# Performance work log

Measured on AMD Instinct MI355X. Metric: run time of the kernel, lower is better.

Reference implementation:

```python
import jax, jax.numpy as jnp
import numpy as np

EMBED = 1024
HEADS = 16
DK = EMBED // HEADS


def setup_inputs() -> dict:
    key = jax.random.key(0)
    ks = jax.random.split(key, 6)
    B, S = 2, 2048
    scale = 1.0 / np.sqrt(EMBED)
    x = jax.random.normal(ks[0], (B, S, EMBED), dtype=jnp.float32)
    Wq = jax.random.normal(ks[1], (EMBED, EMBED), dtype=jnp.float32) * scale
    Wk = jax.random.normal(ks[2], (EMBED, EMBED), dtype=jnp.float32) * scale
    Wv = jax.random.normal(ks[3], (EMBED, EMBED), dtype=jnp.float32) * scale
    Wo = jax.random.normal(ks[4], (EMBED, EMBED), dtype=jnp.float32) * scale
    qw = jnp.zeros((HEADS, 1), dtype=jnp.float32)  # quantum_weight, init quantum_scale=0
    return {"x": x, "Wq": Wq, "Wk": Wk, "Wv": Wv, "Wo": Wo, "qw": qw}


def reference(x, Wq, Wk, Wv, Wo, qw):
    B, S, E = x.shape
    # nn.Linear with no bias: y = x @ W.T; split heads -> [B,H,S,Dk]
    def proj(W):
        return (x @ W.T).reshape(B, S, HEADS, DK).transpose(0, 2, 1, 3)
    q, k, v = proj(Wq), proj(Wk), proj(Wv)
    scores = jnp.einsum('bhsd,bhtd->bhst', q, k) / np.sqrt(DK)
    attn = jax.nn.softmax(scores, axis=-1)  # dropout in eval mode: identity
    classical = jnp.einsum('bhst,bhtd->bhsd', attn, v)
    w = jax.nn.sigmoid(qw)[:, :, None]  # [H,1,1] per-head mixing weight
    out = w * jnp.sin(classical) + (1.0 - w) * classical
    out = out.transpose(0, 2, 1, 3).reshape(B, S, E)
    return out @ Wo.T
```

## Files before the change

### kernel.cpp

```cpp
#include <hip/hip_runtime.h>
#include <math.h>

constexpr int Ec  = 1024;
constexpr int Hc  = 16;
constexpr int DKc = 64;
constexpr int Bc  = 2;
constexpr int Sc  = 2048;
constexpr int Mc  = Bc * Sc;

typedef _Float16 half8 __attribute__((ext_vector_type(8)));
typedef _Float16 half4 __attribute__((ext_vector_type(4)));
typedef float    floatx4  __attribute__((ext_vector_type(4)));
typedef float    floatx16 __attribute__((ext_vector_type(16)));
typedef unsigned int uint2v __attribute__((ext_vector_type(2)));
typedef unsigned int uint4v __attribute__((ext_vector_type(4)));

#define MFMA16(a, b, c) __builtin_amdgcn_mfma_f32_16x16x32_f16(a, b, c, 0, 0, 0)
#define MFMA32(a, b, c) __builtin_amdgcn_mfma_f32_32x32x16_f16(a, b, c, 0, 0, 0)

__device__ __forceinline__ void async_lds16(const _Float16* g, _Float16* l)
{
    __builtin_amdgcn_global_load_lds(
        (const __attribute__((address_space(1))) unsigned int*)g,
        (__attribute__((address_space(3))) unsigned int*)l, 16, 0, 0);
}

__device__ __forceinline__ unsigned pkh2(float a, float b)
{
    return __builtin_bit_cast(unsigned, __builtin_amdgcn_cvt_pkrtz(a, b));
}

__global__ __launch_bounds__(256)
void convert_to_h(const float4* __restrict__ x,
                  const float4* __restrict__ wq,
                  const float4* __restrict__ wk,
                  const float4* __restrict__ wv,
                  const float4* __restrict__ wo,
                  half4* __restrict__ dst)
{
    const int i = blockIdx.x * 256 + threadIdx.x;
    const float4* src; int off;
    if      (i < 1048576) { src = x;  off = i; }
    else if (i < 1310720) { src = wq; off = i - 1048576; }
    else if (i < 1572864) { src = wk; off = i - 1310720; }
    else if (i < 1835008) { src = wv; off = i - 1572864; }
    else                  { src = wo; off = i - 1835008; }
    const float4 v = src[off];
    half4 o;
    o.x = (_Float16)v.x; o.y = (_Float16)v.y;
    o.z = (_Float16)v.z; o.w = (_Float16)v.w;
    dst[i] = o;
}

__device__ __forceinline__ void mfma_gemm_core64(const _Float16* __restrict__ A,
                                                 const _Float16* __restrict__ Bw,
                                                 int m0, int n0,
                                                 _Float16* As, _Float16* Bs,
                                                 floatx4 acc[4][4])
{
    const int tid  = threadIdx.x;
    const int wave = tid >> 6, lane = tid & 63;
    const int l16  = lane & 15, quad = lane >> 4;
    const int wrow = (wave >> 1) * 64, wcol = (wave & 1) * 64;

    const int srow8  = lane >> 3;
    const int schunk = (lane & 7) ^ (srow8 & 7);
    const _Float16* ga = A  + (size_t)(m0 + wave * 32 + srow8) * Ec + schunk * 8;
    const _Float16* gb = Bw + (size_t)(n0 + wave * 32 + srow8) * Ec + schunk * 8;
    _Float16* lA = As + (size_t)(wave * 32) * 64;
    _Float16* lB = Bs + (size_t)(wave * 32) * 64;

    for (int kt = 0; kt < Ec; kt += 64) {
#pragma unroll
        for (int c = 0; c < 4; ++c) {
            async_lds16(ga + (size_t)(c * 8) * Ec + kt, lA + c * 512);
            async_lds16(gb + (size_t)(c * 8) * Ec + kt, lB + c * 512);
        }
        __syncthreads();

        half8 af[4][2], bf[4][2];
#pragma unroll
        for (int i = 0; i < 4; ++i) {
            const int ra = wrow + i * 16 + l16;
            const int rb = wcol + i * 16 + l16;
#pragma unroll
            for (int kc = 0; kc < 2; ++kc) {
                af[i][kc] = *(const half8*)&As[ra * 64 + (((quad + kc * 4) ^ (ra & 7)) * 8)];
                bf[i][kc] = *(const half8*)&Bs[rb * 64 + (((quad + kc * 4) ^ (rb & 7)) * 8)];
            }
        }
#pragma unroll
        for (int i = 0; i < 4; ++i)
#pragma unroll
            for (int j = 0; j < 4; ++j) {
                acc[i][j] = MFMA16(af[i][0], bf[j][0], acc[i][j]);
                acc[i][j] = MFMA16(af[i][1], bf[j][1], acc[i][j]);
            }
        __syncthreads();
    }
}

__global__ __launch_bounds__(256)
void gemm_qkv_fused(const _Float16* __restrict__ xh,
                    const _Float16* __restrict__ wall,
                    _Float16* __restrict__ Qh,
                    _Float16* __restrict__ Kh,
                    _Float16* __restrict__ VTh)
{
    __shared__ __align__(16) _Float16 As[128 * 64];
    __shared__ __align__(16) _Float16 Bs[128 * 64];
    const int lin = blockIdx.x;
    const int swz = (lin & 7) * 96 + (lin >> 3);
    const int m0  = (swz / 24) * 128;
    const int n0f = (swz % 24) * 128;

    floatx4 acc[4][4] = {};
    mfma_gemm_core64(xh, wall, m0, n0f, As, Bs, acc);

    const int tid  = threadIdx.x;
    const int wave = tid >> 6, lane = tid & 63;
    const int l16  = lane & 15, quad = lane >> 4;
    const int wrow = (wave >> 1) * 64, wcol = (wave & 1) * 64;

    const int z   = n0f >> 10;
    const int nl0 = n0f & 1023;

    if (z == 2) {
#pragma unroll
        for (int i = 0; i < 4; ++i)
#pragma unroll
            for (int j = 0; j < 4; ++j) {
                const int n  = nl0 + wcol + j * 16 + l16;
                const int hh = n >> 6, d = n & 63;
                const int mb = m0 + wrow + i * 16 + quad * 4;
                const int bb = mb >> 11, s = mb & (Sc - 1);
                half4 pk;
#pragma unroll
                for (int r = 0; r < 4; ++r) pk[r] = (_Float16)acc[i][j][r];
                *(half4*)&VTh[((size_t)((bb * Hc + hh) * DKc + d)) * Sc + s] = pk;
            }
    } else {
        _Float16* out = (z == 0) ? Qh : Kh;
        const float scale = (z == 0) ? 0.18033688011112042f : 1.0f;
#pragma unroll
        for (int i = 0; i < 4; ++i)
#pragma unroll
            for (int j = 0; j < 4; ++j) {
                const int n = nl0 + wcol + j * 16 + l16;
#pragma unroll
                for (int r = 0; r < 4; ++r) {
                    const int m = m0 + wrow + i * 16 + quad * 4 + r;
                    out[(size_t)m * Ec + n] = (_Float16)(acc[i][j][r] * scale);
                }
            }
    }
}

__global__ __launch_bounds__(256)
void gemm_out_mfma(const _Float16* __restrict__ A,
                   const _Float16* __restrict__ W,
                   float* __restrict__ C)
{
    __shared__ __align__(16) _Float16 As[128 * 64];
    __shared__ __align__(16) _Float16 Bs[64 * 64];
    const int lin = blockIdx.x;
    const int swz = (lin & 7) * 64 + (lin >> 3);
    const int m0 = (swz >> 4) * 128, n0 = (swz & 15) * 64;

    const int tid  = threadIdx.x;
    const int wave = tid >> 6, lane = tid & 63;
    const int l16  = lane & 15, quad = lane >> 4;
    const int wrow = (wave >> 1) * 64, wcol = (wave & 1) * 32;

    const int srow8  = lane >> 3;
    const int schunk = (lane & 7) ^ (srow8 & 7);
    const _Float16* ga = A + (size_t)(m0 + wave * 32 + srow8) * Ec + schunk * 8;
    const _Float16* gb = W + (size_t)(n0 + wave * 16 + srow8) * Ec + schunk * 8;
    _Float16* lA = As + (size_t)(wave * 32) * 64;
    _Float16* lB = Bs + (size_t)(wave * 16) * 64;

    floatx4 acc[4][2] = {};

    for (int kt = 0; kt < Ec; kt += 64) {
#pragma unroll
        for (int c = 0; c < 4; ++c)
            async_lds16(ga + (size_t)(c * 8) * Ec + kt, lA + c * 512);
#pragma unroll
        for (int c = 0; c < 2; ++c)
            async_lds16(gb + (size_t)(c * 8) * Ec + kt, lB + c * 512);
        __syncthreads();

        half8 af[4][2], bf[2][2];
#pragma unroll
        for (int i = 0; i < 4; ++i) {
            const int ra = wrow + i * 16 + l16;
#pragma unroll
            for (int kc = 0; kc < 2; ++kc)
                af[i][kc] = *(const half8*)&As[ra * 64 + (((quad + kc * 4) ^ (ra & 7)) * 8)];
        }
#pragma unroll
        for (int j = 0; j < 2; ++j) {
            const int rb = wcol + j * 16 + l16;
#pragma unroll
            for (int kc = 0; kc < 2; ++kc)
                bf[j][kc] = *(const half8*)&Bs[rb * 64 + (((quad + kc * 4) ^ (rb & 7)) * 8)];
        }
#pragma unroll
        for (int i = 0; i < 4; ++i)
#pragma unroll
            for (int j = 0; j < 2; ++j) {
                acc[i][j] = MFMA16(af[i][0], bf[j][0], acc[i][j]);
                acc[i][j] = MFMA16(af[i][1], bf[j][1], acc[i][j]);
            }
        __syncthreads();
    }

#pragma unroll
    for (int i = 0; i < 4; ++i)
#pragma unroll
        for (int j = 0; j < 2; ++j) {
            const int n = n0 + wcol + j * 16 + l16;
#pragma unroll
            for (int r = 0; r < 4; ++r) {
                const int m = m0 + wrow + i * 16 + quad * 4 + r;
                C[(size_t)m * Ec + n] = acc[i][j][r];
            }
        }
}

__global__ __launch_bounds__(256, 4)
void flash_attn(const _Float16* __restrict__ Qh,
                const _Float16* __restrict__ Kh,
                const _Float16* __restrict__ VTh,
                const float* __restrict__ qw,
                _Float16* __restrict__ Mixh)
{
    constexpr int BM = 128, BN = 64;
    constexpr int NT = Sc / BN;
    __shared__ __align__(16) _Float16 KV[2][2][64 * 64];

    const int tid  = threadIdx.x;
    const int wl   = tid >> 6;
    const int lane = tid & 63;
    const int l31  = lane & 31, hi = lane >> 5;

    const int lin = blockIdx.x;
    const int xcd = lin & 7, idx = lin >> 3;
    const int bh  = xcd * 4 + (idx >> 4);
    const int qx  = idx & 15;
    const int q0  = qx * BM;
    const int h   = bh & (Hc - 1), b = bh >> 4;

    half8 aq[4];
    {
        const _Float16* qp = Qh + (size_t)(b * Sc + q0 + wl * 32 + l31) * Ec
                                + h * DKc + hi * 8;
#pragma unroll
        for (int ks = 0; ks < 4; ++ks) aq[ks] = *(const half8*)(qp + ks * 16);
    }

    const int srow   = lane >> 3;
    const int schunk = (lane & 7) ^ srow;
    const _Float16* Kg = Kh + (size_t)(b * Sc + wl * 16 + srow) * Ec
                            + h * DKc + schunk * 8;
    const _Float16* Vg = VTh + ((size_t)(bh * DKc + wl * 16 + srow)) * Sc
                             + schunk * 8;

    const int xk = l31 & 7;
    const _Float16* kbase[4];
    const _Float16* vbase[4];
#pragma unroll
    for (int ks = 0; ks < 4; ++ks) {
        const int xo = ((((ks << 1) | hi) ^ xk) << 3);
        kbase[ks] = KV[0][0] + l31 * 64 + xo;
        vbase[ks] = KV[0][1] + l31 * 64 + xo;
    }
    _Float16* kd0 = KV[0][0] + (wl * 16) * 64;
    _Float16* vd0 = KV[0][1] + (wl * 16) * 64;

    floatx16 o[2] = {};
    float l_run = 0.f;

    async_lds16(Kg, kd0);
    async_lds16(Kg + (size_t)8 * Ec, kd0 + 512);
    async_lds16(Vg, vd0);
    async_lds16(Vg + (size_t)8 * Sc, vd0 + 512);
    __syncthreads();

    const _Float16* kgp = Kg + (size_t)BN * Ec;
    const _Float16* vgp = Vg + BN;

#define ATTN_TILE(CO)                                                         \
    {                                                                         \
        _Pragma("unroll")                                                     \
        for (int t = 0; t < 2; ++t) {                                         \
            floatx16 st = {};                                                 \
            _Pragma("unroll")                                                 \
            for (int ks = 0; ks < 4; ++ks)                                    \
                st = MFMA32(*(const half8*)(kbase[ks] + (CO) + t * 2048),     \
                            aq[ks], st);                                      \
            float p[16];                                                      \
            _Pragma("unroll")                                                 \
            for (int r = 0; r < 16; ++r) p[r] = __builtin_amdgcn_exp2f(st[r]);\
            float s8[8];                                                      \
            _Pragma("unroll")                                                 \
            for (int r = 0; r < 8; ++r) s8[r] = p[2 * r] + p[2 * r + 1];      \
            float s4[4];                                                      \
            _Pragma("unroll")                                                 \
            for (int r = 0; r < 4; ++r) s4[r] = s8[2 * r] + s8[2 * r + 1];    \
            l_run += ((s4[0] + s4[1]) + (s4[2] + s4[3]));                     \
            half8 pa[2];                                                      \
            _Pragma("unroll")                                                 \
            for (int e = 0; e < 2; ++e) {                                     \
                const unsigned X0 = pkh2(p[8 * e + 0], p[8 * e + 1]);         \
                const unsigned X1 = pkh2(p[8 * e + 2], p[8 * e + 3]);         \
                const unsigned Y0 = pkh2(p[8 * e + 4], p[8 * e + 5]);         \
                const unsigned Y1 = pkh2(p[8 * e + 6], p[8 * e + 7]);         \
                const uint2v s0 = __builtin_amdgcn_permlane32_swap(X0, Y0, false, false); \
                const uint2v s1 = __builtin_amdgcn_permlane32_swap(X1, Y1, false, false); \
                uint4v w; w.x = s0.x; w.y = s1.x; w.z = s0.y; w.w = s1.y;     \
                pa[e] = __builtin_bit_cast(half8, w);                         \
            }                                                                 \
            _Pragma("unroll")                                                 \
            for (int dt = 0; dt < 2; ++dt)                                    \
                _Pragma("unroll")                                             \
                for (int e = 0; e < 2; ++e) {                                 \
                    const half8 bv = *(const half8*)                          \
                        (vbase[2 * t + e] + (CO) + dt * 2048);                \
                    o[dt] = MFMA32(pa[e], bv, o[dt]);                         \
                }                                                             \
        }                                                                     \
    }

    for (int n = 0; n < NT; n += 2) {
        async_lds16(kgp, kd0 + 8192);
        async_lds16(kgp + (size_t)8 * Ec, kd0 + 8192 + 512);
        async_lds16(vgp, vd0 + 8192);
        async_lds16(vgp + (size_t)8 * Sc, vd0 + 8192 + 512);
        kgp += (size_t)BN * Ec; vgp += BN;

        ATTN_TILE(0)
        __syncthreads();

        if (n + 2 < NT) {
            async_lds16(kgp, kd0);
            async_lds16(kgp + (size_t)8 * Ec, kd0 + 512);
            async_lds16(vgp, vd0);
            async_lds16(vgp + (size_t)8 * Sc, vd0 + 512);
            kgp += (size_t)BN * Ec; vgp += BN;
        }

        ATTN_TILE(8192)
        __syncthreads();
    }
#undef ATTN_TILE

    l_run += __shfl_xor(l_run, 32);

    const float wmix = 1.f / (1.f + __expf(-qw[h]));
#pragma unroll
    for (int r = 0; r < 16; ++r) {
        const int row = (r & 3) + 8 * (r >> 2) + 4 * hi;
        const float inv = 1.f / __shfl(l_run, row);
        _Float16* mp = Mixh + (size_t)(b * Sc + q0 + wl * 32 + row) * Ec + h * DKc;
#pragma unroll
        for (int dt = 0; dt < 2; ++dt) {
            const float v = o[dt][r] * inv;
            mp[dt * 32 + l31] = (_Float16)(wmix * __sinf(v) + (1.f - wmix) * v);
        }
    }
}

extern "C" void kernel_launch(void* const* d_in, const int* in_sizes, int n_in,
                              void* d_out, int out_size, void* d_ws, size_t ws_size,
                              hipStream_t stream)
{
    const float* x  = (const float*)d_in[0];
    const float* Wq = (const float*)d_in[1];
    const float* Wk = (const float*)d_in[2];
    const float* Wv = (const float*)d_in[3];
    const float* Wo = (const float*)d_in[4];
    const float* qw = (const float*)d_in[5];
    float* out = (float*)d_out;

    _Float16* hb   = (_Float16*)d_ws;
    _Float16* xh   = hb;
    _Float16* wqh  = hb + (size_t)4 * 1024 * 1024;
    _Float16* woh  = hb + (size_t)7 * 1024 * 1024;
    _Float16* Qh   = hb + (size_t)8 * 1024 * 1024;
    _Float16* Kh   = hb + (size_t)12 * 1024 * 1024;
    _Float16* VTh  = hb + (size_t)16 * 1024 * 1024;
    _Float16* mixh = hb + (size_t)20 * 1024 * 1024;

    convert_to_h<<<dim3(8192), dim3(256), 0, stream>>>(
        (const float4*)x, (const float4*)Wq, (const float4*)Wk,
        (const float4*)Wv, (const float4*)Wo, (half4*)hb);

    gemm_qkv_fused<<<dim3(768), dim3(256), 0, stream>>>(
        xh, wqh, Qh, Kh, VTh);

    flash_attn<<<dim3(512), dim3(256), 0, stream>>>(
        Qh, Kh, VTh, qw, mixh);

    gemm_out_mfma<<<dim3(512), dim3(256), 0, stream>>>(
        mixh, woh, out);
}
```

Baseline: 185.0 us.

## Triple-buffer K/V tiles in flash attention with explicit vmcnt waits

Grows the attention kernel's shared K/V staging from two buffers to three and keeps two tiles in flight ahead of compute. Each step waits on vmcnt for the oldest tile, then issues one barrier instead of two __syncthreads per pair of tiles. The aim is to hide global-to-LDS load latency behind the MFMA work. In exchange, LDS use per block rises from 32KB to 48KB, which may reduce the blocks resident per CU below the launch-bounds target of 4.

```diff
diff --git a/kernel.cpp b/kernel.cpp
--- a/kernel.cpp
+++ b/kernel.cpp
@@ -236,8 +236,7 @@
                 _Float16* __restrict__ Mixh)
 {
     constexpr int BM = 128, BN = 64;
-    constexpr int NT = Sc / BN;
-    __shared__ __align__(16) _Float16 KV[2][2][64 * 64];
+    __shared__ __align__(16) _Float16 KV[3][2][64 * 64];
 
     const int tid  = threadIdx.x;
     const int wl   = tid >> 6;
@@ -261,10 +260,10 @@
 
     const int srow   = lane >> 3;
     const int schunk = (lane & 7) ^ srow;
-    const _Float16* Kg = Kh + (size_t)(b * Sc + wl * 16 + srow) * Ec
-                            + h * DKc + schunk * 8;
-    const _Float16* Vg = VTh + ((size_t)(bh * DKc + wl * 16 + srow)) * Sc
-                             + schunk * 8;
+    const _Float16* kgp = Kh + (size_t)(b * Sc + wl * 16 + srow) * Ec
+                             + h * DKc + schunk * 8;
+    const _Float16* vgp = VTh + ((size_t)(bh * DKc + wl * 16 + srow)) * Sc
+                              + schunk * 8;
 
     const int xk = l31 & 7;
     const _Float16* kbase[4];
@@ -281,14 +280,14 @@
     floatx16 o[2] = {};
     float l_run = 0.f;
 
-    async_lds16(Kg, kd0);
-    async_lds16(Kg + (size_t)8 * Ec, kd0 + 512);
-    async_lds16(Vg, vd0);
-    async_lds16(Vg + (size_t)8 * Sc, vd0 + 512);
-    __syncthreads();
-
-    const _Float16* kgp = Kg + (size_t)BN * Ec;
-    const _Float16* vgp = Vg + BN;
+#define ISSUE_TILE(BUFOFF)                                                    \
+    {                                                                         \
+        async_lds16(kgp, kd0 + (BUFOFF));                                     \
+        async_lds16(kgp + (size_t)8 * Ec, kd0 + (BUFOFF) + 512);              \
+        async_lds16(vgp, vd0 + (BUFOFF));                                     \
+        async_lds16(vgp + (size_t)8 * Sc, vd0 + (BUFOFF) + 512);              \
+        kgp += (size_t)BN * Ec; vgp += BN;                                    \
+    }
 
 #define ATTN_TILE(CO)                                                         \
     {                                                                         \
@@ -332,28 +331,29 @@
         }                                                                     \
     }
 
-    for (int n = 0; n < NT; n += 2) {
-        async_lds16(kgp, kd0 + 8192);
-        async_lds16(kgp + (size_t)8 * Ec, kd0 + 8192 + 512);
-        async_lds16(vgp, vd0 + 8192);
-        async_lds16(vgp + (size_t)8 * Sc, vd0 + 8192 + 512);
-        kgp += (size_t)BN * Ec; vgp += BN;
-
-        ATTN_TILE(0)
-        __syncthreads();
-
-        if (n + 2 < NT) {
-            async_lds16(kgp, kd0);
-            async_lds16(kgp + (size_t)8 * Ec, kd0 + 512);
-            async_lds16(vgp, vd0);
-            async_lds16(vgp + (size_t)8 * Sc, vd0 + 512);
-            kgp += (size_t)BN * Ec; vgp += BN;
-        }
-
-        ATTN_TILE(8192)
-        __syncthreads();
-    }
+#define STEP(TCO, ICO, DO_ISSUE, WN)                                          \
+    {                                                                         \
+        asm volatile("s_waitcnt vmcnt(" #WN ")" ::: "memory");                \
+        __builtin_amdgcn_s_barrier();                                         \
+        __builtin_amdgcn_sched_barrier(0);                                    \
+        if (DO_ISSUE) ISSUE_TILE(ICO);                                        \
+        ATTN_TILE(TCO)                                                        \
+    }
+
+    ISSUE_TILE(0)
+    ISSUE_TILE(8192)
+
+    for (int n = 0; n < 30; n += 3) {
+        STEP(0,     16384, 1, 4)
+        STEP(8192,  0,     1, 4)
+        STEP(16384, 8192,  1, 4)
+    }
+    STEP(0,    0, 0, 4)
+    STEP(8192, 0, 0, 0)
+
+#undef STEP
 #undef ATTN_TILE
+#undef ISSUE_TILE
 
     l_run += __shfl_xor(l_run, 32);
 
```

Measured after the change: 184.8 us. About the same (-0.1%).
